# Optimization experiments

Hardware: AMD Instinct MI355X
Metric: run time of the kernel (lower is better)

The kernel has to match this reference:

```python
import jax, jax.numpy as jnp
import numpy as np

HID = 128   # hidden_size
EDGE = 16   # edge_size
L = 3       # n_layers
K = 3       # sparse_k
U = 4       # atoms per block (uniform)
NB = 20000  # number of blocks
N = NB * U  # number of atoms
EB = 30000  # number of block-level edges


def _egnn_forward(H, Z, edges, edge_attr,
                  emb_in_w, emb_in_b, emb_out_w, emb_out_b,
                  edge_w1, edge_b1, edge_w2, edge_b2,
                  node_w1, node_b1, node_w2, node_b2,
                  coord_w1, coord_b1, coord_w2):
    # ---- sparse-k atom edges from block edges (uniform U atoms per block) ----
    off = jnp.arange(U)
    src_atoms = edges[0][:, None] * U + off            # [EB, U]
    dst_atoms = edges[1][:, None] * U + off            # [EB, U]
    # squared distances between every src/dst atom pair of each block edge
    d2 = jnp.sum((Z[src_atoms][:, :, None, :] - Z[dst_atoms][:, None, :, :]) ** 2, -1)  # [EB,U,U]
    _, idx = jax.lax.top_k(-d2, K)                     # K nearest dst atoms per src atom
    row = jnp.broadcast_to(src_atoms[:, :, None], (EB, U, K)).reshape(-1)   # [E]
    col = jnp.take_along_axis(jnp.broadcast_to(dst_atoms[:, None, :], (EB, U, U)), idx, axis=2).reshape(-1)
    edge_id = jnp.broadcast_to(jnp.arange(EB)[:, None, None], (EB, U, K)).reshape(-1)
    eattr = edge_attr[edge_id]                         # gather block-edge attr per atom edge [E, EDGE]

    # ---- EGNN (Satorras egnn_clean: SiLU, residual h, mean coord agg) ----
    h = H @ emb_in_w + emb_in_b
    x = Z
    ones = jnp.ones((row.shape[0], 1), Z.dtype)
    cnt = jnp.clip(jax.ops.segment_sum(ones, row, num_segments=N), 1.0)
    for l in range(L):
        diff = x[row] - x[col]                         # [E,3]
        radial = jnp.sum(diff * diff, -1, keepdims=True)
        m = jnp.concatenate([h[row], h[col], radial, eattr], -1)   # [E, 2*HID+1+EDGE]
        m = jax.nn.silu(m @ edge_w1[l] + edge_b1[l])
        m = jax.nn.silu(m @ edge_w2[l] + edge_b2[l])   # edge messages [E, HID]
        # coordinate update (mean aggregation over outgoing edges of row)
        w = jax.nn.silu(m @ coord_w1[l] + coord_b1[l]) @ coord_w2[l]   # [E,1]
        x = x + jax.ops.segment_sum(diff * w, row, num_segments=N) / cnt
        # node update (sum aggregation, residual)
        agg = jax.ops.segment_sum(m, row, num_segments=N)
        hn = jnp.concatenate([h, agg], -1)
        h = h + (jax.nn.silu(hn @ node_w1[l] + node_b1[l]) @ node_w2[l] + node_b2[l])
    h = h @ emb_out_w + emb_out_b
    return h, x


def setup_inputs() -> dict:
    key = jax.random.key(0)
    ks = jax.random.split(key, 16)
    s = 0.05
    p = {}
    p["H"] = jax.random.normal(ks[0], (N, HID), jnp.float32)
    p["Z"] = jax.random.normal(ks[1], (N, 3), jnp.float32) * 3.0
    p["block_id"] = jnp.repeat(jnp.arange(NB, dtype=jnp.int32), U)
    p["batch_id"] = jnp.zeros((N,), jnp.int32)
    p["edges"] = jax.random.randint(ks[2], (2, EB), 0, NB, dtype=jnp.int32)
    p["edge_attr"] = jax.random.normal(ks[3], (EB, EDGE), jnp.float32)
    p["emb_in_w"] = jax.random.normal(ks[4], (HID, HID), jnp.float32) * s
    p["emb_in_b"] = jnp.zeros((HID,), jnp.float32)
    p["emb_out_w"] = jax.random.normal(ks[5], (HID, HID), jnp.float32) * s
    p["emb_out_b"] = jnp.zeros((HID,), jnp.float32)
    p["edge_w1"] = jax.random.normal(ks[6], (L, 2 * HID + 1 + EDGE, HID), jnp.float32) * s
    p["edge_b1"] = jnp.zeros((L, HID), jnp.float32)
    p["edge_w2"] = jax.random.normal(ks[7], (L, HID, HID), jnp.float32) * s
    p["edge_b2"] = jnp.zeros((L, HID), jnp.float32)
    p["node_w1"] = jax.random.normal(ks[8], (L, 2 * HID, HID), jnp.float32) * s
    p["node_b1"] = jnp.zeros((L, HID), jnp.float32)
    p["node_w2"] = jax.random.normal(ks[9], (L, HID, HID), jnp.float32) * s
    p["node_b2"] = jnp.zeros((L, HID), jnp.float32)
    p["coord_w1"] = jax.random.normal(ks[10], (L, HID, HID), jnp.float32) * s
    p["coord_b1"] = jnp.zeros((L, HID), jnp.float32)
    p["coord_w2"] = jax.random.normal(ks[11], (L, HID, 1), jnp.float32) * s
    return p


def reference(H, Z, block_id, batch_id, edges, edge_attr,
              emb_in_w, emb_in_b, emb_out_w, emb_out_b,
              edge_w1, edge_b1, edge_w2, edge_b2,
              node_w1, node_b1, node_w2, node_b2,
              coord_w1, coord_b1, coord_w2):
    # block_id / batch_id are carried for API fidelity; uniform-U block layout is static.
    return _egnn_forward(H, Z, edges, edge_attr,
                         emb_in_w, emb_in_b, emb_out_w, emb_out_b,
                         edge_w1, edge_b1, edge_w2, edge_b2,
                         node_w1, node_b1, node_w2, node_b2,
                         coord_w1, coord_b1, coord_w2)
```

## Files before the change

kernel.cpp:

```cpp
#include <hip/hip_runtime.h>
#include <math.h>

#define HIDC 128
#define EDGEF 16
#define LAY 3
#define KNN 3
#define UU 4
#define NBLK 20000
#define NATOM (NBLK*UU)
#define EBK 30000
#define EALL (EBK*UU*KNN)
#define NGRP (EBK*UU)

#define W1F_L 36864
#define W2F_L 16384
#define NW1F_L 32768

#define E_WG 16
#define ROWS_WG (E_WG*12)
#define WAVES_WG 12

typedef __attribute__((ext_vector_type(8))) short bf16x8;
typedef __attribute__((ext_vector_type(4))) float f32x4;

__device__ __forceinline__ float silu_f(float v) {
    return __fdividef(v, 1.0f + __expf(-v));
}

__device__ __forceinline__ unsigned short f2bf(float f) {
    union { float f; unsigned int u; } v; v.f = f;
    unsigned int r = v.u + 0x7FFFu + ((v.u >> 16) & 1u);
    return (unsigned short)(r >> 16);
}

__device__ __forceinline__ float bf2f(unsigned short h) {
    union { unsigned int u; float f; } t; t.u = ((unsigned int)h) << 16;
    return t.f;
}

__device__ __forceinline__ void split2(float v, short& hi, short& lo) {
    unsigned short h = f2bf(v);
    hi = (short)h;
    lo = (short)f2bf(v - bf2f(h));
}

__device__ __forceinline__ void csplit(float v, unsigned short& hi, unsigned short& lo) {
    unsigned int hu = __float_as_uint(v) & 0xffff0000u;
    hi = (unsigned short)(hu >> 16);
    lo = f2bf(v - __uint_as_float(hu));
}

__device__ __forceinline__ unsigned int packhl(float v) {
    unsigned int hu = __float_as_uint(v) & 0xffff0000u;
    return hu | (unsigned int)f2bf(v - __uint_as_float(hu));
}

__device__ __forceinline__ float unpackf(unsigned int u) {
    return bf2f((unsigned short)(u >> 16)) + bf2f((unsigned short)(u & 0xffffu));
}

__device__ __forceinline__ void unpack8(uint4 v0, uint4 v1, bf16x8& ah, bf16x8& al) {
    unsigned int uu[8] = {v0.x, v0.y, v0.z, v0.w, v1.x, v1.y, v1.z, v1.w};
    #pragma unroll
    for (int q = 0; q < 8; q++) {
        ah[q] = (short)(unsigned short)(uu[q] >> 16);
        al[q] = (short)(unsigned short)(uu[q] & 0xffffu);
    }
}

__device__ __forceinline__ void stage16(const unsigned short* gsrc, unsigned short* ldst) {
    __builtin_amdgcn_global_load_lds(
        (const __attribute__((address_space(1))) unsigned int*)(const void*)gsrc,
        (__attribute__((address_space(3))) unsigned int*)(void*)ldst,
        16, 0, 0);
}


__global__ void k_count(const int* __restrict__ edges, int* __restrict__ degB) {
    int e = blockIdx.x * 256 + threadIdx.x;
    if (e < EBK) atomicAdd(&degB[edges[e]], 1);
}

__global__ void k_scan(const int* __restrict__ degB, int* __restrict__ offB) {
    __shared__ int s[1024];
    __shared__ int carry;
    if (threadIdx.x == 0) carry = 0;
    __syncthreads();
    for (int base = 0; base < NBLK; base += 1024) {
        int i = base + threadIdx.x;
        int v = (i < NBLK) ? degB[i] : 0;
        s[threadIdx.x] = v;
        __syncthreads();
        for (int d = 1; d < 1024; d <<= 1) {
            int t = (threadIdx.x >= d) ? s[threadIdx.x - d] : 0;
            __syncthreads();
            s[threadIdx.x] += t;
            __syncthreads();
        }
        if (i < NBLK) offB[i] = carry + s[threadIdx.x] - v;
        int tot = s[1023];
        __syncthreads();
        if (threadIdx.x == 0) carry += tot;
        __syncthreads();
    }
    if (threadIdx.x == 0) offB[NBLK] = carry;
}

__global__ void k_fill(const int* __restrict__ edges, const int* __restrict__ offB,
                       int* __restrict__ cursor, int* __restrict__ listE) {
    int e = blockIdx.x * 256 + threadIdx.x;
    if (e < EBK) {
        int b = edges[e];
        int p = atomicAdd(&cursor[b], 1);
        listE[offB[b] + p] = e;
    }
}

__global__ void k_topk(const int* __restrict__ edges, const float* __restrict__ Z,
                       int* __restrict__ colIdx) {
    int t = blockIdx.x * 256 + threadIdx.x;
    if (t >= EBK * UU) return;
    int e = t >> 2, u = t & 3;
    int b0 = edges[e], b1 = edges[EBK + e];
    int s = b0 * UU + u;
    float zs0 = Z[s*3+0], zs1 = Z[s*3+1], zs2 = Z[s*3+2];
    float d2[UU];
    #pragma unroll
    for (int v = 0; v < UU; v++) {
        int d = b1 * UU + v;
        float a0 = __fsub_rn(zs0, Z[d*3+0]);
        float a1 = __fsub_rn(zs1, Z[d*3+1]);
        float a2 = __fsub_rn(zs2, Z[d*3+2]);
        float p0 = __fmul_rn(a0, a0);
        float p1 = __fmul_rn(a1, a1);
        float p2 = __fmul_rn(a2, a2);
        d2[v] = __fadd_rn(__fadd_rn(p0, p1), p2);
    }
    bool used[UU] = {false, false, false, false};
    #pragma unroll
    for (int k = 0; k < KNN; k++) {
        int best = -1;
        float bd = INFINITY;
        #pragma unroll
        for (int v = 0; v < UU; v++) {
            if (!used[v] && d2[v] < bd) { bd = d2[v]; best = v; }
        }
        used[best] = true;
        colIdx[t * KNN + k] = b1 * UU + best;
    }
}


__global__ void k_wfrag(const float* __restrict__ ew1, const float* __restrict__ ew2,
                        const float* __restrict__ cw1,
                        const float* __restrict__ nw1, const float* __restrict__ nw2,
                        unsigned short* __restrict__ w1f_hi, unsigned short* __restrict__ w1f_lo,
                        unsigned short* __restrict__ w2f_hi, unsigned short* __restrict__ w2f_lo,
                        unsigned short* __restrict__ c1f_hi, unsigned short* __restrict__ c1f_lo,
                        unsigned short* __restrict__ n1f_hi, unsigned short* __restrict__ n1f_lo,
                        unsigned short* __restrict__ n2f_hi, unsigned short* __restrict__ n2f_lo) {
    int i = blockIdx.x * 256 + threadIdx.x;
    float v = 0.f;
    unsigned short* dh = nullptr;
    unsigned short* dl = nullptr;
    int di = 0;
    if (i < 3 * W1F_L) {
        int l = i / W1F_L, rem = i % W1F_L;
        int chunk = rem >> 9, lane = (rem >> 3) & 63, t = rem & 7;
        int kb = chunk >> 3, j = chunk & 7;
        int k = kb*32 + (lane >> 4)*8 + t, n = j*16 + (lane & 15);
        v = (k < 273) ? ew1[(size_t)l*273*128 + (size_t)k*128 + n] : 0.f;
        dh = w1f_hi; dl = w1f_lo; di = i;
    } else {
        int i2 = i - 3 * W1F_L;
        if (i2 < 3 * W2F_L) {
            int l = i2 / W2F_L, rem = i2 % W2F_L;
            int chunk = rem >> 9, lane = (rem >> 3) & 63, t = rem & 7;
            int kb = chunk >> 3, j = chunk & 7;
            int k = kb*32 + (lane >> 4)*8 + t, n = j*16 + (lane & 15);
            v = ew2[(size_t)l*128*128 + (size_t)k*128 + n];
            dh = w2f_hi; dl = w2f_lo; di = i2;
        } else {
            int i3 = i2 - 3 * W2F_L;
            if (i3 < 3 * W2F_L) {
                int l = i3 / W2F_L, rem = i3 % W2F_L;
                int chunk = rem >> 9, lane = (rem >> 3) & 63, t = rem & 7;
                int kb = chunk >> 3, j = chunk & 7;
                int k = kb*32 + (lane >> 4)*8 + t, n = j*16 + (lane & 15);
                v = cw1[(size_t)l*128*128 + (size_t)k*128 + n];
                dh = c1f_hi; dl = c1f_lo; di = i3;
            } else {
                int i4 = i3 - 3 * W2F_L;
                if (i4 < 3 * NW1F_L) {
                    int l = i4 / NW1F_L, rem = i4 % NW1F_L;
                    int chunk = rem >> 9, lane = (rem >> 3) & 63, t = rem & 7;
                    int kb = chunk >> 3, j = chunk & 7;
                    int k = kb*32 + (lane >> 4)*8 + t, n = j*16 + (lane & 15);
                    v = nw1[(size_t)l*256*128 + (size_t)k*128 + n];
                    dh = n1f_hi; dl = n1f_lo; di = i4;
                } else {
                    int i5 = i4 - 3 * NW1F_L;
                    if (i5 >= 3 * W2F_L) return;
                    int l = i5 / W2F_L, rem = i5 % W2F_L;
                    int chunk = rem >> 9, lane = (rem >> 3) & 63, t = rem & 7;
                    int kb = chunk >> 3, j = chunk & 7;
                    int k = kb*32 + (lane >> 4)*8 + t, n = j*16 + (lane & 15);
                    v = nw2[(size_t)l*128*128 + (size_t)k*128 + n];
                    dh = n2f_hi; dl = n2f_lo; di = i5;
                }
            }
        }
    }
    short hi, lo;
    split2(v, hi, lo);
    dh[di] = (unsigned short)hi;
    dl[di] = (unsigned short)lo;
}


__global__ __launch_bounds__(768, 6) void k_edge_flat(
    const unsigned int* __restrict__ hp,
    const float* __restrict__ x,
    const float* __restrict__ eattr,
    const int* __restrict__ edges0,
    const int* __restrict__ colIdx,
    const unsigned short* __restrict__ w1f_hi, const unsigned short* __restrict__ w1f_lo,
    const unsigned short* __restrict__ w2f_hi, const unsigned short* __restrict__ w2f_lo,
    const unsigned short* __restrict__ c1f_hi, const unsigned short* __restrict__ c1f_lo,
    const float* __restrict__ eb1,
    const float* __restrict__ eb2,
    const float* __restrict__ cb1,
    const float* __restrict__ cw2v,
    unsigned short* __restrict__ msum,
    float* __restrict__ xsum)
{
    __shared__ unsigned short wbufH[4096], wbufL[4096];
    __shared__ unsigned short Mlds[ROWS_WG * 128];
    __shared__ float diffLDS[ROWS_WG][3];
    __shared__ float pLDS[ROWS_WG];

    const int tid = threadIdx.x;
    const int wid = tid >> 6, l = tid & 63;
    const int g = l >> 4, er = l & 15;
    const int e_base = blockIdx.x * E_WG;
    const int r0 = wid * 16;

    const int row_g = r0 + er;
    const int e_loc = row_g / 12;
    const int rr = row_g - e_loc * 12;
    const int u = rr / 3;
    const int kk = rr - u * 3;
    const int e = e_base + e_loc;
    const int bs = edges0[e];
    const int srcA = bs * 4 + u;
    const int colA = colIdx[(e * 4 + u) * 3 + kk];
    float rad = 0.f;
    if (g == 0) {
        float dx = x[srcA*3+0] - x[colA*3+0];
        float dy = x[srcA*3+1] - x[colA*3+1];
        float dz = x[srcA*3+2] - x[colA*3+2];
        rad = dx*dx + dy*dy + dz*dz;
        diffLDS[row_g][0] = dx; diffLDS[row_g][1] = dy; diffLDS[row_g][2] = dz;
    }

    const int goff = wid * 512 + l * 8;
    unsigned short* lb0H = wbufH + wid * 512;
    unsigned short* lb1H = wbufH + 2048 + wid * 512;
    unsigned short* lb0L = wbufL + wid * 512;
    unsigned short* lb1L = wbufL + 2048 + wid * 512;

    {
        f32x4 acc[8];
        #pragma unroll
        for (int jj = 0; jj < 8; jj++) acc[jj] = (f32x4){0.f, 0.f, 0.f, 0.f};

        #pragma unroll 1
        for (int kb = 0; kb < 9; kb++) {
            __syncthreads();
            if (wid < 4) {
                stage16(w1f_hi + (kb << 12) + goff,        lb0H);
                stage16(w1f_hi + (kb << 12) + 2048 + goff, lb1H);
                stage16(w1f_lo + (kb << 12) + goff,        lb0L);
                stage16(w1f_lo + (kb << 12) + 2048 + goff, lb1L);
            }
            bf16x8 ah, al;
            if (kb < 8) {
                const unsigned int* src = (kb < 4) ? (hp + (size_t)srcA * 128 + kb * 32 + g * 8)
                                                   : (hp + (size_t)colA * 128 + (kb - 4) * 32 + g * 8);
                uint4 v0 = *(const uint4*)src;
                uint4 v1 = *((const uint4*)src + 1);
                unpack8(v0, v1, ah, al);
            } else {
                float tv[8];
                #pragma unroll
                for (int q = 0; q < 8; q++) tv[q] = 0.f;
                if (g == 0) {
                    tv[0] = rad;
                    #pragma unroll
                    for (int q = 1; q < 8; q++) tv[q] = eattr[(size_t)e*16 + (q-1)];
                } else if (g == 1) {
                    #pragma unroll
                    for (int q = 0; q < 8; q++) tv[q] = eattr[(size_t)e*16 + 7 + q];
                } else if (g == 2) {
                    tv[0] = eattr[(size_t)e*16 + 15];
                }
                #pragma unroll
                for (int q = 0; q < 8; q++) { unsigned short hh, ll; csplit(tv[q], hh, ll); ah[q] = (short)hh; al[q] = (short)ll; }
            }
            __syncthreads();
            __builtin_amdgcn_s_setprio(1);
            #pragma unroll
            for (int jj = 0; jj < 8; jj++) {
                const int off = (jj << 9) + (l << 3);
                bf16x8 wh = *(const bf16x8*)&wbufH[off];
                bf16x8 wl = *(const bf16x8*)&wbufL[off];
                acc[jj] = __builtin_amdgcn_mfma_f32_16x16x32_bf16(ah, wh, acc[jj], 0, 0, 0);
                acc[jj] = __builtin_amdgcn_mfma_f32_16x16x32_bf16(al, wh, acc[jj], 0, 0, 0);
                acc[jj] = __builtin_amdgcn_mfma_f32_16x16x32_bf16(ah, wl, acc[jj], 0, 0, 0);
            }
            __builtin_amdgcn_s_setprio(0);
        }
        #pragma unroll
        for (int jj = 0; jj < 8; jj++) {
            const int n = jj * 16 + er;
            const float bv = eb1[n];
            #pragma unroll
            for (int reg = 0; reg < 4; reg++) {
                const int row = r0 + g * 4 + reg;
                float v = silu_f(acc[jj][reg] + bv);
                Mlds[row * 128 + (n ^ ((row & 7) << 3))] = f2bf(v);
            }
        }
    }

    {
        f32x4 acc[8];
        #pragma unroll
        for (int jj = 0; jj < 8; jj++) acc[jj] = (f32x4){0.f, 0.f, 0.f, 0.f};

        #pragma unroll 1
        for (int kb = 0; kb < 4; kb++) {
            __syncthreads();
            if (wid < 4) {
                stage16(w2f_hi + (kb << 12) + goff,        lb0H);
                stage16(w2f_hi + (kb << 12) + 2048 + goff, lb1H);
                stage16(w2f_lo + (kb << 12) + goff,        lb0L);
                stage16(w2f_lo + (kb << 12) + 2048 + goff, lb1L);
            }
            const int aoff = row_g * 128 + ((kb * 32 + g * 8) ^ ((row_g & 7) << 3));
            bf16x8 a2 = *(const bf16x8*)&Mlds[aoff];
            __syncthreads();
            __builtin_amdgcn_s_setprio(1);
            #pragma unroll
            for (int jj = 0; jj < 8; jj++) {
                const int off = (jj << 9) + (l << 3);
                bf16x8 wh = *(const bf16x8*)&wbufH[off];
                bf16x8 wl = *(const bf16x8*)&wbufL[off];
                acc[jj] = __builtin_amdgcn_mfma_f32_16x16x32_bf16(a2, wh, acc[jj], 0, 0, 0);
                acc[jj] = __builtin_amdgcn_mfma_f32_16x16x32_bf16(a2, wl, acc[jj], 0, 0, 0);
            }
            __builtin_amdgcn_s_setprio(0);
        }
        #pragma unroll
        for (int jj = 0; jj < 8; jj++) {
            const int n = jj * 16 + er;
            const float bv = eb2[n];
            #pragma unroll
            for (int reg = 0; reg < 4; reg++) {
                const int row = r0 + g * 4 + reg;
                float v = silu_f(acc[jj][reg] + bv);
                Mlds[row * 128 + (n ^ ((row & 7) << 3))] = f2bf(v);
            }
        }
    }
    __syncthreads();

    {
        const int col = tid & 127;
        const int gslot = tid >> 7;
        for (int gi = gslot; gi < E_WG * 4; gi += 6) {
            const int el = gi >> 2, uu2 = gi & 3;
            const int base = el * 12 + uu2 * 3;
            float ms = 0.f;
            #pragma unroll
            for (int k3 = 0; k3 < 3; k3++) {
                const int row = base + k3;
                ms += bf2f(Mlds[row * 128 + (col ^ ((row & 7) << 3))]);
            }
            msum[(size_t)((e_base + el) * 4 + uu2) * 128 + col] = f2bf(ms);
        }
    }

    {
        f32x4 acc[8];
        #pragma unroll
        for (int jj = 0; jj < 8; jj++) acc[jj] = (f32x4){0.f, 0.f, 0.f, 0.f};

        #pragma unroll 1
        for (int kb = 0; kb < 4; kb++) {
            __syncthreads();
            if (wid < 4) {
                stage16(c1f_hi + (kb << 12) + goff,        lb0H);
                stage16(c1f_hi + (kb << 12) + 2048 + goff, lb1H);
                stage16(c1f_lo + (kb << 12) + goff,        lb0L);
                stage16(c1f_lo + (kb << 12) + 2048 + goff, lb1L);
            }
            const int aoff = row_g * 128 + ((kb * 32 + g * 8) ^ ((row_g & 7) << 3));
            bf16x8 a3 = *(const bf16x8*)&Mlds[aoff];
            __syncthreads();
            __builtin_amdgcn_s_setprio(1);
            #pragma unroll
            for (int jj = 0; jj < 8; jj++) {
                const int off = (jj << 9) + (l << 3);
                bf16x8 wh = *(const bf16x8*)&wbufH[off];
                bf16x8 wl = *(const bf16x8*)&wbufL[off];
                acc[jj] = __builtin_amdgcn_mfma_f32_16x16x32_bf16(a3, wh, acc[jj], 0, 0, 0);
                acc[jj] = __builtin_amdgcn_mfma_f32_16x16x32_bf16(a3, wl, acc[jj], 0, 0, 0);
            }
            __builtin_amdgcn_s_setprio(0);
        }
        float p[4] = {0.f, 0.f, 0.f, 0.f};
        #pragma unroll
        for (int jj = 0; jj < 8; jj++) {
            const int n = jj * 16 + er;
            const float cb = cb1[n], cw = cw2v[n];
            #pragma unroll
            for (int reg = 0; reg < 4; reg++)
                p[reg] += silu_f(acc[jj][reg] + cb) * cw;
        }
        #pragma unroll
        for (int d = 1; d < 16; d <<= 1) {
            #pragma unroll
            for (int reg = 0; reg < 4; reg++)
                p[reg] += __shfl_xor(p[reg], d);
        }
        if (er == 0) {
            #pragma unroll
            for (int reg = 0; reg < 4; reg++)
                pLDS[r0 + g * 4 + reg] = p[reg];
        }
    }
    __syncthreads();

    if (tid < E_WG * 4 * 3) {
        const int gi = tid / 3, c = tid - gi * 3;
        const int el = gi >> 2, uu2 = gi & 3;
        const int base = el * 12 + uu2 * 3;
        float xs = 0.f;
        #pragma unroll
        for (int k3 = 0; k3 < 3; k3++)
            xs += diffLDS[base + k3][c] * pLDS[base + k3];
        xsum[(size_t)((e_base + el) * 4 + uu2) * 3 + c] = xs;
    }
}


__global__ void k_xupd(const float* __restrict__ xcur, const float* __restrict__ xsum,
                       const int* __restrict__ offB, const int* __restrict__ listE,
                       float* __restrict__ xnext)
{
    int i = blockIdx.x * 256 + threadIdx.x;
    if (i >= NATOM * 3) return;
    int a = i / 3, d = i - a * 3;
    int b = a >> 2, u = a & 3;
    int o0 = offB[b], o1 = offB[b + 1];
    float xs = 0.f;
    for (int pos = o0; pos < o1; pos++) {
        int e = listE[pos];
        xs += xsum[(size_t)(e * 4 + u) * 3 + d];
    }
    int deg = o1 - o0;
    xnext[i] = xcur[i] + ((deg > 0) ? xs / (3.0f * (float)deg) : 0.f);
}


__global__ __launch_bounds__(256, 4) void k_node(
    unsigned int* __restrict__ hp,
    const unsigned short* __restrict__ msum,
    const int* __restrict__ offB,
    const int* __restrict__ listE,
    const unsigned short* __restrict__ n1f_hi, const unsigned short* __restrict__ n1f_lo,
    const unsigned short* __restrict__ n2f_hi, const unsigned short* __restrict__ n2f_lo,
    const float* __restrict__ nb1,
    const float* __restrict__ nb2)
{
    __shared__ unsigned short wbufH[4096], wbufL[4096];
    __shared__ unsigned short hid[4][16 * 128];

    const int tid = threadIdx.x;
    const int wid = tid >> 6, l = tid & 63;
    const int g = l >> 4, er = l & 15;
    const int a0 = blockIdx.x * 64 + wid * 16;
    const int a = a0 + er;
    const int b = a >> 2, u = a & 3;
    const int o0 = offB[b], o1 = offB[b + 1];

    const int goff = wid * 512 + l * 8;
    unsigned short* lb0H = wbufH + wid * 512;
    unsigned short* lb1H = wbufH + 2048 + wid * 512;
    unsigned short* lb0L = wbufL + wid * 512;
    unsigned short* lb1L = wbufL + 2048 + wid * 512;

    {
        f32x4 acc[8];
        #pragma unroll
        for (int jj = 0; jj < 8; jj++) acc[jj] = (f32x4){0.f, 0.f, 0.f, 0.f};

        #pragma unroll 1
        for (int kb = 0; kb < 8; kb++) {
            __syncthreads();
            stage16(n1f_hi + (kb << 12) + goff,        lb0H);
            stage16(n1f_hi + (kb << 12) + 2048 + goff, lb1H);
            stage16(n1f_lo + (kb << 12) + goff,        lb0L);
            stage16(n1f_lo + (kb << 12) + 2048 + goff, lb1L);
            bf16x8 ah, al;
            if (kb < 4) {
                const unsigned int* src = hp + (size_t)a * 128 + kb * 32 + g * 8;
                uint4 v0 = *(const uint4*)src;
                uint4 v1 = *((const uint4*)src + 1);
                unpack8(v0, v1, ah, al);
            } else {
                float s[8];
                #pragma unroll
                for (int q = 0; q < 8; q++) s[q] = 0.f;
                for (int pos = o0; pos < o1; pos++) {
                    const int e = listE[pos];
                    bf16x8 mv = *(const bf16x8*)(msum + (size_t)(e * 4 + u) * 128 + (kb - 4) * 32 + g * 8);
                    #pragma unroll
                    for (int q = 0; q < 8; q++) s[q] += bf2f((unsigned short)mv[q]);
                }
                #pragma unroll
                for (int q = 0; q < 8; q++) { unsigned short hh, ll; csplit(s[q], hh, ll); ah[q] = (short)hh; al[q] = (short)ll; }
            }
            __syncthreads();
            __builtin_amdgcn_s_setprio(1);
            #pragma unroll
            for (int jj = 0; jj < 8; jj++) {
                const int off = (jj << 9) + (l << 3);
                bf16x8 wh = *(const bf16x8*)&wbufH[off];
                bf16x8 wl = *(const bf16x8*)&wbufL[off];
                acc[jj] = __builtin_amdgcn_mfma_f32_16x16x32_bf16(ah, wh, acc[jj], 0, 0, 0);
                acc[jj] = __builtin_amdgcn_mfma_f32_16x16x32_bf16(al, wh, acc[jj], 0, 0, 0);
                acc[jj] = __builtin_amdgcn_mfma_f32_16x16x32_bf16(ah, wl, acc[jj], 0, 0, 0);
            }
            __builtin_amdgcn_s_setprio(0);
        }
        #pragma unroll
        for (int jj = 0; jj < 8; jj++) {
            const int n = jj * 16 + er;
            const float bv = nb1[n];
            #pragma unroll
            for (int reg = 0; reg < 4; reg++) {
                const int row = g * 4 + reg;
                float v = silu_f(acc[jj][reg] + bv);
                hid[wid][row * 128 + (n ^ ((row & 7) << 3))] = f2bf(v);
            }
        }
    }

    {
        f32x4 acc[8];
        #pragma unroll
        for (int jj = 0; jj < 8; jj++) acc[jj] = (f32x4){0.f, 0.f, 0.f, 0.f};

        #pragma unroll 1
        for (int kb = 0; kb < 4; kb++) {
            __syncthreads();
            stage16(n2f_hi + (kb << 12) + goff,        lb0H);
            stage16(n2f_hi + (kb << 12) + 2048 + goff, lb1H);
            stage16(n2f_lo + (kb << 12) + goff,        lb0L);
            stage16(n2f_lo + (kb << 12) + 2048 + goff, lb1L);
            const int aoff = er * 128 + ((kb * 32 + g * 8) ^ ((er & 7) << 3));
            bf16x8 ab = *(const bf16x8*)&hid[wid][aoff];
            __syncthreads();
            __builtin_amdgcn_s_setprio(1);
            #pragma unroll
            for (int jj = 0; jj < 8; jj++) {
                const int off = (jj << 9) + (l << 3);
                bf16x8 wh = *(const bf16x8*)&wbufH[off];
                bf16x8 wl = *(const bf16x8*)&wbufL[off];
                acc[jj] = __builtin_amdgcn_mfma_f32_16x16x32_bf16(ab, wh, acc[jj], 0, 0, 0);
                acc[jj] = __builtin_amdgcn_mfma_f32_16x16x32_bf16(ab, wl, acc[jj], 0, 0, 0);
            }
            __builtin_amdgcn_s_setprio(0);
        }
        #pragma unroll
        for (int jj = 0; jj < 8; jj++) {
            const int n = jj * 16 + er;
            const float bv = nb2[n];
            #pragma unroll
            for (int reg = 0; reg < 4; reg++) {
                const int row = g * 4 + reg;
                const size_t idx = (size_t)(a0 + row) * 128 + n;
                float v = acc[jj][reg] + bv + unpackf(hp[idx]);
                hp[idx] = packhl(v);
            }
        }
    }
}


template<int KT, bool PACKIN, bool PACKOUT>
__global__ __launch_bounds__(128) void k_gemm(
    const float* __restrict__ A0,
    const float* __restrict__ W, const float* __restrict__ bias,
    float* __restrict__ C, int M)
{
    __shared__ float At[KT][32];
    __shared__ float Bs[32][128];
    const int tid = threadIdx.x;
    const int tile0 = blockIdx.x * 32;
    const int r = tid >> 2, part = tid & 3;
    const int gr = tile0 + r;

    if (gr < M) {
        #pragma unroll
        for (int j = 0; j < 8; j++) {
            int c = part * 32 + j * 4;
            float f0, f1, f2, f3;
            if (PACKIN) {
                const unsigned int* ap = (const unsigned int*)A0 + (size_t)gr * 128 + c;
                uint4 v = *(const uint4*)ap;
                f0 = unpackf(v.x); f1 = unpackf(v.y); f2 = unpackf(v.z); f3 = unpackf(v.w);
            } else {
                float4 v = *(const float4*)(A0 + (size_t)gr * 128 + c);
                f0 = v.x; f1 = v.y; f2 = v.z; f3 = v.w;
            }
            At[c][r] = f0; At[c+1][r] = f1; At[c+2][r] = f2; At[c+3][r] = f3;
        }
    } else {
        #pragma unroll
        for (int j = 0; j < 8; j++) {
            int c = part * 32 + j * 4;
            At[c][r] = 0.f; At[c+1][r] = 0.f; At[c+2][r] = 0.f; At[c+3][r] = 0.f;
        }
    }

    float acc[4][8];
    #pragma unroll
    for (int i = 0; i < 4; i++)
        #pragma unroll
        for (int j = 0; j < 8; j++) acc[i][j] = 0.f;

    const int tx = tid & 15, ty = tid >> 4;

    for (int kb = 0; kb < KT / 32; kb++) {
        __syncthreads();
        #pragma unroll
        for (int j = 0; j < 8; j++) {
            int li = j * 512 + tid * 4;
            int kk = li >> 7, c = li & 127;
            float4 v = *(const float4*)(W + (size_t)(kb * 32 + kk) * 128 + c);
            *(float4*)&Bs[kk][c] = v;
        }
        __syncthreads();
        #pragma unroll 8
        for (int kk = 0; kk < 32; kk++) {
            float4 a  = *(const float4*)&At[kb * 32 + kk][ty * 4];
            float4 b0 = *(const float4*)&Bs[kk][tx * 8];
            float4 b1 = *(const float4*)&Bs[kk][tx * 8 + 4];
            float av[4] = {a.x, a.y, a.z, a.w};
            float bv[8] = {b0.x, b0.y, b0.z, b0.w, b1.x, b1.y, b1.z, b1.w};
            #pragma unroll
            for (int i = 0; i < 4; i++)
                #pragma unroll
                for (int j = 0; j < 8; j++)
                    acc[i][j] = fmaf(av[i], bv[j], acc[i][j]);
        }
    }

    #pragma unroll
    for (int i = 0; i < 4; i++) {
        int grr = tile0 + ty * 4 + i;
        if (grr >= M) continue;
        #pragma unroll
        for (int j = 0; j < 8; j++) {
            int c = tx * 8 + j;
            float v = acc[i][j] + bias[c];
            if (PACKOUT) ((unsigned int*)C)[(size_t)grr * 128 + c] = packhl(v);
            else         C[(size_t)grr * 128 + c] = v;
        }
    }
}


extern "C" void kernel_launch(void* const* d_in, const int* in_sizes, int n_in,
                              void* d_out, int out_size, void* d_ws, size_t ws_size,
                              hipStream_t stream) {
    const float* H        = (const float*)d_in[0];
    const float* Z        = (const float*)d_in[1];
    const int*   edges    = (const int*)  d_in[4];
    const float* eattr    = (const float*)d_in[5];
    const float* emb_in_w = (const float*)d_in[6];
    const float* emb_in_b = (const float*)d_in[7];
    const float* emb_out_w= (const float*)d_in[8];
    const float* emb_out_b= (const float*)d_in[9];
    const float* edge_w1  = (const float*)d_in[10];
    const float* edge_b1  = (const float*)d_in[11];
    const float* edge_w2  = (const float*)d_in[12];
    const float* edge_b2  = (const float*)d_in[13];
    const float* node_w1  = (const float*)d_in[14];
    const float* node_b1  = (const float*)d_in[15];
    const float* node_w2  = (const float*)d_in[16];
    const float* node_b2  = (const float*)d_in[17];
    const float* coord_w1 = (const float*)d_in[18];
    const float* coord_b1 = (const float*)d_in[19];
    const float* coord_w2 = (const float*)d_in[20];

    float* out  = (float*)d_out;
    float* hbuf = out;
    unsigned int* hp = (unsigned int*)hbuf;
    float* xout = out + (size_t)NATOM * 128;

    char* w = (char*)d_ws;
    unsigned short* msum = (unsigned short*)w;  w += (size_t)NGRP * 128 * 2;
    float* xsum = (float*)w;           w += (size_t)NGRP * 3 * 4;
    float* xA  = (float*)w;            w += (size_t)NATOM * 3 * 4;
    float* xB  = (float*)w;            w += (size_t)NATOM * 3 * 4;
    unsigned short* w1f_hi = (unsigned short*)w;  w += (size_t)3 * W1F_L * 2;
    unsigned short* w1f_lo = (unsigned short*)w;  w += (size_t)3 * W1F_L * 2;
    unsigned short* w2f_hi = (unsigned short*)w;  w += (size_t)3 * W2F_L * 2;
    unsigned short* w2f_lo = (unsigned short*)w;  w += (size_t)3 * W2F_L * 2;
    unsigned short* c1f_hi = (unsigned short*)w;  w += (size_t)3 * W2F_L * 2;
    unsigned short* c1f_lo = (unsigned short*)w;  w += (size_t)3 * W2F_L * 2;
    unsigned short* n1f_hi = (unsigned short*)w;  w += (size_t)3 * NW1F_L * 2;
    unsigned short* n1f_lo = (unsigned short*)w;  w += (size_t)3 * NW1F_L * 2;
    unsigned short* n2f_hi = (unsigned short*)w;  w += (size_t)3 * W2F_L * 2;
    unsigned short* n2f_lo = (unsigned short*)w;  w += (size_t)3 * W2F_L * 2;
    int* colIdx = (int*)w;             w += (size_t)EALL * 4;
    int* degB   = (int*)w;             w += (size_t)NBLK * 4;
    int* cursor = (int*)w;             w += (size_t)NBLK * 4;
    int* listE  = (int*)w;             w += (size_t)EBK * 4;
    int* offB   = (int*)w;             w += (size_t)(NBLK + 1) * 4;

    hipMemsetAsync(degB,   0, NBLK * sizeof(int), stream);
    hipMemsetAsync(cursor, 0, NBLK * sizeof(int), stream);

    k_count<<<(EBK + 255) / 256, 256, 0, stream>>>(edges, degB);
    k_scan <<<1, 1024, 0, stream>>>(degB, offB);
    k_fill <<<(EBK + 255) / 256, 256, 0, stream>>>(edges, offB, cursor, listE);
    k_topk <<<(EBK * UU + 255) / 256, 256, 0, stream>>>(edges, Z, colIdx);

    {
        int total = 3 * W1F_L + 3 * W2F_L + 3 * W2F_L + 3 * NW1F_L + 3 * W2F_L;
        k_wfrag<<<(total + 255) / 256, 256, 0, stream>>>(
            edge_w1, edge_w2, coord_w1, node_w1, node_w2,
            w1f_hi, w1f_lo, w2f_hi, w2f_lo, c1f_hi, c1f_lo,
            n1f_hi, n1f_lo, n2f_hi, n2f_lo);
    }

    k_gemm<128, false, true><<<NATOM / 32, 128, 0, stream>>>(
        H, emb_in_w, emb_in_b, (float*)hp, NATOM);

    const float* xcur = Z;
    for (int l = 0; l < LAY; l++) {
        float* xnext = (l == 0) ? xA : (l == 1) ? xB : xout;

        k_edge_flat<<<EBK / E_WG, 768, 0, stream>>>(
            hp, xcur, eattr, edges, colIdx,
            w1f_hi + (size_t)l * W1F_L, w1f_lo + (size_t)l * W1F_L,
            w2f_hi + (size_t)l * W2F_L, w2f_lo + (size_t)l * W2F_L,
            c1f_hi + (size_t)l * W2F_L, c1f_lo + (size_t)l * W2F_L,
            edge_b1 + l * 128, edge_b2 + l * 128, coord_b1 + l * 128, coord_w2 + l * 128,
            msum, xsum);

        k_xupd<<<(NATOM * 3 + 255) / 256, 256, 0, stream>>>(xcur, xsum, offB, listE, xnext);

        k_node<<<NATOM / 64, 256, 0, stream>>>(
            hp, msum, offB, listE,
            n1f_hi + (size_t)l * NW1F_L, n1f_lo + (size_t)l * NW1F_L,
            n2f_hi + (size_t)l * W2F_L, n2f_lo + (size_t)l * W2F_L,
            node_b1 + l * 128, node_b2 + l * 128);

        xcur = xnext;
    }

    k_gemm<128, true, false><<<NATOM / 32, 128, 0, stream>>>(
        hbuf, emb_out_w, emb_out_b, hbuf, NATOM);
}
```

Before: 895.7 us.

## Store hidden state as separate bf16 hi/lo planes and pack epilogue conversions

Replaces the interleaved packed hi|lo 32-bit hidden-state layout with two separate bf16 planes in workspace, so MFMA operands load directly as bf16x8 vectors without per-element unpacking. Epilogues convert pairs of outputs with the hardware packed bf16 conversion instruction. The message-sum reduction is moved later in the kernel and now processes two columns per thread with 32-bit LDS reads and stores. The cost is extra workspace and two separate memory streams for the hidden state.

Result: slower. 918.7 us (+2.6%).

```diff
diff --git a/kernel.cpp b/kernel.cpp
--- a/kernel.cpp
+++ b/kernel.cpp
@@ -50,22 +50,10 @@
     lo = f2bf(v - __uint_as_float(hu));
 }
 
-__device__ __forceinline__ unsigned int packhl(float v) {
-    unsigned int hu = __float_as_uint(v) & 0xffff0000u;
-    return hu | (unsigned int)f2bf(v - __uint_as_float(hu));
-}
-
-__device__ __forceinline__ float unpackf(unsigned int u) {
-    return bf2f((unsigned short)(u >> 16)) + bf2f((unsigned short)(u & 0xffffu));
-}
-
-__device__ __forceinline__ void unpack8(uint4 v0, uint4 v1, bf16x8& ah, bf16x8& al) {
-    unsigned int uu[8] = {v0.x, v0.y, v0.z, v0.w, v1.x, v1.y, v1.z, v1.w};
-    #pragma unroll
-    for (int q = 0; q < 8; q++) {
-        ah[q] = (short)(unsigned short)(uu[q] >> 16);
-        al[q] = (short)(unsigned short)(uu[q] & 0xffffu);
-    }
+__device__ __forceinline__ unsigned int cvtpk2(float a, float b) {
+    unsigned int r;
+    asm("v_cvt_pk_bf16_f32 %0, %1, %2" : "=v"(r) : "v"(a), "v"(b));
+    return r;
 }
 
 __device__ __forceinline__ void stage16(const unsigned short* gsrc, unsigned short* ldst) {
@@ -219,7 +207,8 @@
 
 
 __global__ __launch_bounds__(768, 6) void k_edge_flat(
-    const unsigned int* __restrict__ hp,
+    const unsigned short* __restrict__ hHI,
+    const unsigned short* __restrict__ hLO,
     const float* __restrict__ x,
     const float* __restrict__ eattr,
     const int* __restrict__ edges0,
@@ -285,11 +274,10 @@
             }
             bf16x8 ah, al;
             if (kb < 8) {
-                const unsigned int* src = (kb < 4) ? (hp + (size_t)srcA * 128 + kb * 32 + g * 8)
-                                                   : (hp + (size_t)colA * 128 + (kb - 4) * 32 + g * 8);
-                uint4 v0 = *(const uint4*)src;
-                uint4 v1 = *((const uint4*)src + 1);
-                unpack8(v0, v1, ah, al);
+                const size_t off = (kb < 4) ? ((size_t)srcA * 128 + kb * 32 + g * 8)
+                                            : ((size_t)colA * 128 + (kb - 4) * 32 + g * 8);
+                ah = *(const bf16x8*)(hHI + off);
+                al = *(const bf16x8*)(hLO + off);
             } else {
                 float tv[8];
                 #pragma unroll
@@ -321,14 +309,18 @@
             __builtin_amdgcn_s_setprio(0);
         }
         #pragma unroll
-        for (int jj = 0; jj < 8; jj++) {
-            const int n = jj * 16 + er;
-            const float bv = eb1[n];
+        for (int jp = 0; jp < 4; jp++) {
+            const int n0 = (jp * 2) * 16 + er, n1 = n0 + 16;
+            const float b0 = eb1[n0], b1 = eb1[n1];
             #pragma unroll
             for (int reg = 0; reg < 4; reg++) {
                 const int row = r0 + g * 4 + reg;
-                float v = silu_f(acc[jj][reg] + bv);
-                Mlds[row * 128 + (n ^ ((row & 7) << 3))] = f2bf(v);
+                float v0 = silu_f(acc[jp*2][reg] + b0);
+                float v1 = silu_f(acc[jp*2+1][reg] + b1);
+                unsigned int pk = cvtpk2(v0, v1);
+                const int m = (row & 7) << 3;
+                Mlds[row * 128 + (n0 ^ m)] = (unsigned short)pk;
+                Mlds[row * 128 + (n1 ^ m)] = (unsigned short)(pk >> 16);
             }
         }
     }
@@ -362,32 +354,19 @@
             __builtin_amdgcn_s_setprio(0);
         }
         #pragma unroll
-        for (int jj = 0; jj < 8; jj++) {
-            const int n = jj * 16 + er;
-            const float bv = eb2[n];
+        for (int jp = 0; jp < 4; jp++) {
+            const int n0 = (jp * 2) * 16 + er, n1 = n0 + 16;
+            const float b0 = eb2[n0], b1 = eb2[n1];
             #pragma unroll
             for (int reg = 0; reg < 4; reg++) {
                 const int row = r0 + g * 4 + reg;
-                float v = silu_f(acc[jj][reg] + bv);
-                Mlds[row * 128 + (n ^ ((row & 7) << 3))] = f2bf(v);
-            }
-        }
-    }
-    __syncthreads();
-
-    {
-        const int col = tid & 127;
-        const int gslot = tid >> 7;
-        for (int gi = gslot; gi < E_WG * 4; gi += 6) {
-            const int el = gi >> 2, uu2 = gi & 3;
-            const int base = el * 12 + uu2 * 3;
-            float ms = 0.f;
-            #pragma unroll
-            for (int k3 = 0; k3 < 3; k3++) {
-                const int row = base + k3;
-                ms += bf2f(Mlds[row * 128 + (col ^ ((row & 7) << 3))]);
-            }
-            msum[(size_t)((e_base + el) * 4 + uu2) * 128 + col] = f2bf(ms);
+                float v0 = silu_f(acc[jp*2][reg] + b0);
+                float v1 = silu_f(acc[jp*2+1][reg] + b1);
+                unsigned int pk = cvtpk2(v0, v1);
+                const int m = (row & 7) << 3;
+                Mlds[row * 128 + (n0 ^ m)] = (unsigned short)pk;
+                Mlds[row * 128 + (n1 ^ m)] = (unsigned short)(pk >> 16);
+            }
         }
     }
 
@@ -442,6 +421,22 @@
     }
     __syncthreads();
 
+    for (int t = tid; t < E_WG * 4 * 64; t += 768) {
+        const int gi = t >> 6, cp = t & 63;
+        const int c0 = cp * 2;
+        const int el = gi >> 2, uu2 = gi & 3;
+        const int base = el * 12 + uu2 * 3;
+        float s0 = 0.f, s1 = 0.f;
+        #pragma unroll
+        for (int k3 = 0; k3 < 3; k3++) {
+            const int row = base + k3;
+            const int m = (row & 7) << 3;
+            unsigned int pr = *(const unsigned int*)&Mlds[row * 128 + (c0 ^ m)];
+            s0 += bf2f((unsigned short)(pr & 0xffffu));
+            s1 += bf2f((unsigned short)(pr >> 16));
+        }
+        ((unsigned int*)msum)[(size_t)((e_base + el) * 4 + uu2) * 64 + cp] = cvtpk2(s0, s1);
+    }
     if (tid < E_WG * 4 * 3) {
         const int gi = tid / 3, c = tid - gi * 3;
         const int el = gi >> 2, uu2 = gi & 3;
@@ -475,7 +470,8 @@
 
 
 __global__ __launch_bounds__(256, 4) void k_node(
-    unsigned int* __restrict__ hp,
+    unsigned short* __restrict__ hHI,
+    unsigned short* __restrict__ hLO,
     const unsigned short* __restrict__ msum,
     const int* __restrict__ offB,
     const int* __restrict__ listE,
@@ -515,10 +511,9 @@
             stage16(n1f_lo + (kb << 12) + 2048 + goff, lb1L);
             bf16x8 ah, al;
             if (kb < 4) {
-                const unsigned int* src = hp + (size_t)a * 128 + kb * 32 + g * 8;
-                uint4 v0 = *(const uint4*)src;
-                uint4 v1 = *((const uint4*)src + 1);
-                unpack8(v0, v1, ah, al);
+                const size_t off = (size_t)a * 128 + kb * 32 + g * 8;
+                ah = *(const bf16x8*)(hHI + off);
+                al = *(const bf16x8*)(hLO + off);
             } else {
                 float s[8];
                 #pragma unroll
@@ -546,14 +541,18 @@
             __builtin_amdgcn_s_setprio(0);
         }
         #pragma unroll
-        for (int jj = 0; jj < 8; jj++) {
-            const int n = jj * 16 + er;
-            const float bv = nb1[n];
+        for (int jp = 0; jp < 4; jp++) {
+            const int n0 = (jp * 2) * 16 + er, n1 = n0 + 16;
+            const float b0 = nb1[n0], b1 = nb1[n1];
             #pragma unroll
             for (int reg = 0; reg < 4; reg++) {
                 const int row = g * 4 + reg;
-                float v = silu_f(acc[jj][reg] + bv);
-                hid[wid][row * 128 + (n ^ ((row & 7) << 3))] = f2bf(v);
+                float v0 = silu_f(acc[jp*2][reg] + b0);
+                float v1 = silu_f(acc[jp*2+1][reg] + b1);
+                unsigned int pk = cvtpk2(v0, v1);
+                const int m = (row & 7) << 3;
+                hid[wid][row * 128 + (n0 ^ m)] = (unsigned short)pk;
+                hid[wid][row * 128 + (n1 ^ m)] = (unsigned short)(pk >> 16);
             }
         }
     }
@@ -592,21 +591,25 @@
             for (int reg = 0; reg < 4; reg++) {
                 const int row = g * 4 + reg;
                 const size_t idx = (size_t)(a0 + row) * 128 + n;
-                float v = acc[jj][reg] + bv + unpackf(hp[idx]);
-                hp[idx] = packhl(v);
-            }
-        }
-    }
-}
-
-
-template<int KT, bool PACKIN, bool PACKOUT>
+                float v = acc[jj][reg] + bv + bf2f(hHI[idx]) + bf2f(hLO[idx]);
+                unsigned short hh, ll; csplit(v, hh, ll);
+                hHI[idx] = hh;
+                hLO[idx] = ll;
+            }
+        }
+    }
+}
+
+
+template<bool PLANEIN, bool PLANEOUT>
 __global__ __launch_bounds__(128) void k_gemm(
     const float* __restrict__ A0,
+    const unsigned short* __restrict__ AHI, const unsigned short* __restrict__ ALO,
     const float* __restrict__ W, const float* __restrict__ bias,
-    float* __restrict__ C, int M)
+    float* __restrict__ C,
+    unsigned short* __restrict__ CHI, unsigned short* __restrict__ CLO, int M)
 {
-    __shared__ float At[KT][32];
+    __shared__ float At[128][32];
     __shared__ float Bs[32][128];
     const int tid = threadIdx.x;
     const int tile0 = blockIdx.x * 32;
@@ -618,10 +621,13 @@
         for (int j = 0; j < 8; j++) {
             int c = part * 32 + j * 4;
             float f0, f1, f2, f3;
-            if (PACKIN) {
-                const unsigned int* ap = (const unsigned int*)A0 + (size_t)gr * 128 + c;
-                uint4 v = *(const uint4*)ap;
-                f0 = unpackf(v.x); f1 = unpackf(v.y); f2 = unpackf(v.z); f3 = unpackf(v.w);
+            if (PLANEIN) {
+                ushort4 vh = *(const ushort4*)(AHI + (size_t)gr * 128 + c);
+                ushort4 vl = *(const ushort4*)(ALO + (size_t)gr * 128 + c);
+                f0 = bf2f(vh.x) + bf2f(vl.x);
+                f1 = bf2f(vh.y) + bf2f(vl.y);
+                f2 = bf2f(vh.z) + bf2f(vl.z);
+                f3 = bf2f(vh.w) + bf2f(vl.w);
             } else {
                 float4 v = *(const float4*)(A0 + (size_t)gr * 128 + c);
                 f0 = v.x; f1 = v.y; f2 = v.z; f3 = v.w;
@@ -644,7 +650,7 @@
 
     const int tx = tid & 15, ty = tid >> 4;
 
-    for (int kb = 0; kb < KT / 32; kb++) {
+    for (int kb = 0; kb < 4; kb++) {
         __syncthreads();
         #pragma unroll
         for (int j = 0; j < 8; j++) {
@@ -677,8 +683,13 @@
         for (int j = 0; j < 8; j++) {
             int c = tx * 8 + j;
             float v = acc[i][j] + bias[c];
-            if (PACKOUT) ((unsigned int*)C)[(size_t)grr * 128 + c] = packhl(v);
-            else         C[(size_t)grr * 128 + c] = v;
+            if (PLANEOUT) {
+                unsigned short hh, ll; csplit(v, hh, ll);
+                CHI[(size_t)grr * 128 + c] = hh;
+                CLO[(size_t)grr * 128 + c] = ll;
+            } else {
+                C[(size_t)grr * 128 + c] = v;
+            }
         }
     }
 }
@@ -709,11 +720,12 @@
 
     float* out  = (float*)d_out;
     float* hbuf = out;
-    unsigned int* hp = (unsigned int*)hbuf;
     float* xout = out + (size_t)NATOM * 128;
 
     char* w = (char*)d_ws;
-    unsigned short* msum = (unsigned short*)w;  w += (size_t)NGRP * 128 * 2;
+    unsigned short* hHI = (unsigned short*)w;  w += (size_t)NATOM * 128 * 2;
+    unsigned short* hLO = (unsigned short*)w;  w += (size_t)NATOM * 128 * 2;
+    unsigned short* msum = (unsigned short*)w; w += (size_t)NGRP * 128 * 2;
     float* xsum = (float*)w;           w += (size_t)NGRP * 3 * 4;
     float* xA  = (float*)w;            w += (size_t)NATOM * 3 * 4;
     float* xB  = (float*)w;            w += (size_t)NATOM * 3 * 4;
@@ -749,15 +761,15 @@
             n1f_hi, n1f_lo, n2f_hi, n2f_lo);
     }
 
-    k_gemm<128, false, true><<<NATOM / 32, 128, 0, stream>>>(
-        H, emb_in_w, emb_in_b, (float*)hp, NATOM);
+    k_gemm<false, true><<<NATOM / 32, 128, 0, stream>>>(
+        H, nullptr, nullptr, emb_in_w, emb_in_b, nullptr, hHI, hLO, NATOM);
 
     const float* xcur = Z;
     for (int l = 0; l < LAY; l++) {
         float* xnext = (l == 0) ? xA : (l == 1) ? xB : xout;
 
         k_edge_flat<<<EBK / E_WG, 768, 0, stream>>>(
-            hp, xcur, eattr, edges, colIdx,
+            hHI, hLO, xcur, eattr, edges, colIdx,
             w1f_hi + (size_t)l * W1F_L, w1f_lo + (size_t)l * W1F_L,
             w2f_hi + (size_t)l * W2F_L, w2f_lo + (size_t)l * W2F_L,
             c1f_hi + (size_t)l * W2F_L, c1f_lo + (size_t)l * W2F_L,
@@ -767,7 +779,7 @@
         k_xupd<<<(NATOM * 3 + 255) / 256, 256, 0, stream>>>(xcur, xsum, offB, listE, xnext);
 
         k_node<<<NATOM / 64, 256, 0, stream>>>(
-            hp, msum, offB, listE,
+            hHI, hLO, msum, offB, listE,
             n1f_hi + (size_t)l * NW1F_L, n1f_lo + (size_t)l * NW1F_L,
             n2f_hi + (size_t)l * W2F_L, n2f_lo + (size_t)l * W2F_L,
             node_b1 + l * 128, node_b2 + l * 128);
@@ -775,6 +787,6 @@
         xcur = xnext;
     }
 
-    k_gemm<128, true, false><<<NATOM / 32, 128, 0, stream>>>(
-        hbuf, emb_out_w, emb_out_b, hbuf, NATOM);
-}
+    k_gemm<true, false><<<NATOM / 32, 128, 0, stream>>>(
+        nullptr, hHI, hLO, emb_out_w, emb_out_b, hbuf, nullptr, nullptr, NATOM);
+}
```
